# Optimization experiments

Measured on AMD Instinct MI355X. Metric: run time of the kernel, lower is better.

Reference implementation:

```python
import jax, jax.numpy as jnp
import numpy as np

N = 131072
F_IN = 256
FEATURES = 64
N_SOURCES = 32


def setup_inputs() -> dict:
    key = jax.random.key(0)
    k1, k2, k3 = jax.random.split(key, 3)
    x = jax.random.normal(k1, (N, F_IN), dtype=jnp.float32)
    source = jax.random.randint(k2, (N,), 0, N_SOURCES, dtype=jnp.int32)
    W = jax.random.normal(k3, (F_IN, N_SOURCES * FEATURES), dtype=jnp.float32) * (1.0 / np.sqrt(F_IN))
    b = jnp.zeros((N_SOURCES * FEATURES,), dtype=jnp.float32)
    return {"x": x, "source": source, "W": W, "b": b}


def reference(x, source, W, b):
    # Dense projection to all sources: (N, n_sources*features)
    y = jnp.dot(x, W) + b
    # Per-row gather of the slice belonging to this row's source id.
    # Equivalent to y[i, source[i]*FEATURES : (source[i]+1)*FEATURES].
    y = y.reshape(x.shape[0], N_SOURCES, FEATURES)
    out = jnp.take_along_axis(y, source[:, None, None].astype(jnp.int32), axis=1)
    return out[:, 0, :]  # (N, FEATURES)
```

## Files before the change

### kernel.cpp

```cpp
#include <hip/hip_runtime.h>

#define N_ROWS   131072
#define F_IN     256
#define FEAT     64
#define NSRC     32
#define WSTRIDE  (NSRC * FEAT)
#define NCH      32
#define CHUNK    4096
#define LCAP     320
#define NBUCK    (NCH * NSRC)
#define KPAD     264
#define TPAD     66
#define TR       32

#define MCHUNK   4096
#define LCAP1    512

typedef __attribute__((ext_vector_type(8))) short  bf16x8;
typedef __attribute__((ext_vector_type(4))) float  f32x4;

__device__ __forceinline__ unsigned short f2bf(float f) {
    union { float f; unsigned u; } c; c.f = f;
    unsigned r = c.u + 0x7fffu + ((c.u >> 16) & 1u);
    return (unsigned short)(r >> 16);
}

__device__ __forceinline__ bf16x8 pack8(f32x4 f0, f32x4 f1) {
    bf16x8 a;
    a[0] = (short)f2bf(f0[0]); a[1] = (short)f2bf(f0[1]);
    a[2] = (short)f2bf(f0[2]); a[3] = (short)f2bf(f0[3]);
    a[4] = (short)f2bf(f1[0]); a[5] = (short)f2bf(f1[1]);
    a[6] = (short)f2bf(f1[2]); a[7] = (short)f2bf(f1[3]);
    return a;
}

__global__ void zero_counts(int* __restrict__ ws) {
    const int i = blockIdx.x * 256 + threadIdx.x;
    if (i < NBUCK) ws[i] = 0;
}

__global__ __launch_bounds__(256)
void compact_kernel(const int* __restrict__ src, int* __restrict__ ws) {
    __shared__ int lcnt[NSRC];
    __shared__ int gbase[NSRC];
    const int tid = threadIdx.x;
    if (tid < NSRC) lcnt[tid] = 0;
    __syncthreads();
    const int row = blockIdx.x * 256 + tid;
    const int s   = src[row];
    const int c   = blockIdx.x >> 4;
    const int p   = atomicAdd(&lcnt[s], 1);
    __syncthreads();
    if (tid < NSRC && lcnt[tid] > 0)
        gbase[tid] = atomicAdd(&ws[c * NSRC + tid], lcnt[tid]);
    __syncthreads();
    const int pos = gbase[s] + p;
    if (pos < LCAP)
        ws[NBUCK + ((size_t)(c * NSRC + s)) * LCAP + pos] = row;
}

__device__ __forceinline__ void load_tile(const float* __restrict__ x,
                                          const int* lst, int count, int tile,
                                          int row8, int p, f32x4 av[8]) {
    const int gi  = min(tile * TR + row8, count - 1);
    const int row = lst[gi];
    const float* rp = x + (size_t)row * F_IN + p * 4;
    #pragma unroll
    for (int i = 0; i < 8; ++i)
        av[i] = *(const f32x4*)(rp + i * 32);
}

__device__ __forceinline__ void write_tile(unsigned short* XsBuf,
                                           int row8, int p, const f32x4 av[8]) {
    #pragma unroll
    for (int i = 0; i < 8; ++i) {
        unsigned lo = (unsigned)f2bf(av[i][0]) | ((unsigned)f2bf(av[i][1]) << 16);
        unsigned hi = (unsigned)f2bf(av[i][2]) | ((unsigned)f2bf(av[i][3]) << 16);
        unsigned* d = (unsigned*)&XsBuf[row8 * KPAD + i * 32 + p * 4];
        d[0] = lo; d[1] = hi;
    }
}

__device__ __forceinline__ void tile_compute(
    const unsigned short* __restrict__ XsBuf, const unsigned short* __restrict__ Wt,
    float* __restrict__ T, const int* __restrict__ lst,
    float bias0, float bias1, float* __restrict__ out,
    int tile, int count, int w, int lane, int col, int quad, int mh, int nh) {

    f32x4 acc0 = (f32x4){0.f, 0.f, 0.f, 0.f};
    f32x4 acc1 = (f32x4){0.f, 0.f, 0.f, 0.f};
    #pragma unroll
    for (int kk = 0; kk < 8; ++kk) {
        const bf16x8 a = *(const bf16x8*)&XsBuf[(mh * 16 + col) * KPAD + kk * 32 + quad * 8];
        const bf16x8 b0 = *(const bf16x8*)&Wt[(nh * 32 + col) * KPAD + kk * 32 + quad * 8];
        const bf16x8 b1 = *(const bf16x8*)&Wt[(nh * 32 + 16 + col) * KPAD + kk * 32 + quad * 8];
        acc0 = __builtin_amdgcn_mfma_f32_16x16x32_bf16(a, b0, acc0, 0, 0, 0);
        acc1 = __builtin_amdgcn_mfma_f32_16x16x32_bf16(a, b1, acc1, 0, 0, 0);
    }
    #pragma unroll
    for (int reg = 0; reg < 4; ++reg) {
        T[(mh * 16 + quad * 4 + reg) * TPAD + nh * 32 + col]      = acc0[reg] + bias0;
        T[(mh * 16 + quad * 4 + reg) * TPAD + nh * 32 + 16 + col] = acc1[reg] + bias1;
    }
    __syncthreads();
    #pragma unroll
    for (int r = 0; r < 8; ++r) {
        const int lr = w * 8 + r;
        const int gi = tile * TR + lr;
        if (gi < count) {
            const int grow = lst[gi];
            out[(size_t)grow * FEAT + lane] = T[lr * TPAD + lane];
        }
    }
}

__global__ __launch_bounds__(256, 2)
void gemm_kernel(const float* __restrict__ x, const float* __restrict__ W,
                 const float* __restrict__ b, const int* __restrict__ ws,
                 float* __restrict__ out) {
    __shared__ __align__(16) unsigned short Wt[FEAT * KPAD];
    __shared__ __align__(16) unsigned short Xs[2][TR * KPAD];
    __shared__ __align__(16) float T[TR * TPAD];
    __shared__ int lst[LCAP];

    const int tid    = threadIdx.x;
    const int c      = blockIdx.x;
    const int s      = blockIdx.y;
    const int bucket = c * NSRC + s;
    const int count  = min(ws[bucket], LCAP);
    if (count == 0) return;

    const int* gl = ws + NBUCK + (size_t)bucket * LCAP;
    for (int i = tid; i < count; i += 256) lst[i] = gl[i];

    {
        const int n  = tid & 63;
        const int kp = (tid >> 6) * 2;
        #pragma unroll
        for (int k0 = 0; k0 < F_IN; k0 += 8) {
            const int k = k0 + kp;
            const float w0 = W[(size_t)k       * WSTRIDE + s * FEAT + n];
            const float w1 = W[(size_t)(k + 1) * WSTRIDE + s * FEAT + n];
            *(unsigned*)&Wt[n * KPAD + k] = (unsigned)f2bf(w0) | ((unsigned)f2bf(w1) << 16);
        }
    }

    const int lane = tid & 63, w = tid >> 6;
    const int col  = lane & 15, quad = lane >> 4;
    const int mh   = w & 1,    nh   = w >> 1;
    const int row8 = tid >> 3, p    = tid & 7;

    const float bias0 = b[s * FEAT + nh * 32 + col];
    const float bias1 = b[s * FEAT + nh * 32 + 16 + col];

    __syncthreads();

    const int ntiles = (count + TR - 1) / TR;
    f32x4 avA[8], avB[8];
    load_tile(x, lst, count, 0, row8, p, avA);

    for (int t = 0; t < ntiles; t += 2) {
        write_tile(Xs[0], row8, p, avA);
        if (t + 1 < ntiles) load_tile(x, lst, count, t + 1, row8, p, avB);
        __syncthreads();
        tile_compute(Xs[0], Wt, T, lst, bias0, bias1, out,
                     t, count, w, lane, col, quad, mh, nh);
        if (t + 1 >= ntiles) break;

        write_tile(Xs[1], row8, p, avB);
        if (t + 2 < ntiles) load_tile(x, lst, count, t + 2, row8, p, avA);
        __syncthreads();
        tile_compute(Xs[1], Wt, T, lst, bias0, bias1, out,
                     t + 1, count, w, lane, col, quad, mh, nh);
    }
}

__global__ __launch_bounds__(256, 4)
void mono_kernel(const float* __restrict__ x, const int* __restrict__ src,
                 const float* __restrict__ W, const float* __restrict__ b,
                 float* __restrict__ out) {
    __shared__ __align__(16) unsigned short Wt[FEAT * KPAD];
    __shared__ int lst[LCAP1];
    __shared__ int cnt;
    const int tid = threadIdx.x, s = blockIdx.y, chunk0 = blockIdx.x * MCHUNK;
    if (tid == 0) cnt = 0;
    __syncthreads();
    {
        const int n = tid & 63, kp = (tid >> 6) * 2;
        #pragma unroll
        for (int k0 = 0; k0 < F_IN; k0 += 8) {
            const int k = k0 + kp;
            const float w0 = W[(size_t)k * WSTRIDE + s * FEAT + n];
            const float w1 = W[(size_t)(k + 1) * WSTRIDE + s * FEAT + n];
            *(unsigned*)&Wt[n * KPAD + k] = (unsigned)f2bf(w0) | ((unsigned)f2bf(w1) << 16);
        }
    }
    #pragma unroll
    for (int r = 0; r < MCHUNK / 256; ++r) {
        const int row = chunk0 + r * 256 + tid;
        if (src[row] == s) {
            const int p = atomicAdd(&cnt, 1);
            if (p < LCAP1) lst[p] = row;
        }
    }
    __syncthreads();
    const int count = cnt;
    if (count == 0) return;
    const int lane = tid & 63, w = tid >> 6, col = lane & 15, quad = lane >> 4;
    float bias[4];
    #pragma unroll
    for (int nt = 0; nt < 4; ++nt) bias[nt] = b[s * FEAT + nt * 16 + col];
    const int npass = (count + 63) >> 6;
    for (int pp = 0; pp < npass; ++pp) {
        const int base = pp * 64 + w * 16;
        const int ia = lst[min(base + col, count - 1)];
        const float* ap = x + (size_t)ia * F_IN + quad * 8;
        f32x4 av[16];
        #pragma unroll
        for (int kk = 0; kk < 8; ++kk) {
            av[2 * kk]     = *(const f32x4*)(ap + kk * 32);
            av[2 * kk + 1] = *(const f32x4*)(ap + kk * 32 + 4);
        }
        f32x4 acc[4];
        #pragma unroll
        for (int nt = 0; nt < 4; ++nt) acc[nt] = (f32x4){0.f, 0.f, 0.f, 0.f};
        #pragma unroll
        for (int kk = 0; kk < 8; ++kk) {
            const bf16x8 a = pack8(av[2 * kk], av[2 * kk + 1]);
            #pragma unroll
            for (int nt = 0; nt < 4; ++nt) {
                const bf16x8 bb = *(const bf16x8*)&Wt[(nt * 16 + col) * KPAD + kk * 32 + quad * 8];
                acc[nt] = __builtin_amdgcn_mfma_f32_16x16x32_bf16(a, bb, acc[nt], 0, 0, 0);
            }
        }
        #pragma unroll
        for (int reg = 0; reg < 4; ++reg) {
            const int gm = base + quad * 4 + reg;
            if (gm < count) {
                const int row = lst[gm];
                float* op = out + (size_t)row * FEAT;
                #pragma unroll
                for (int nt = 0; nt < 4; ++nt)
                    op[nt * 16 + col] = acc[nt][reg] + bias[nt];
            }
        }
    }
}

extern "C" void kernel_launch(void* const* d_in, const int* in_sizes, int n_in,
                              void* d_out, int out_size, void* d_ws, size_t ws_size,
                              hipStream_t stream) {
    const float* x   = (const float*)d_in[0];
    const int*   src = (const int*)d_in[1];
    const float* W   = (const float*)d_in[2];
    const float* b   = (const float*)d_in[3];
    float*       out = (float*)d_out;

    const size_t ws_needed = (size_t)NBUCK * (1 + LCAP) * sizeof(int);
    if (ws_size >= ws_needed) {
        int* ws = (int*)d_ws;
        zero_counts<<<dim3(4), dim3(256), 0, stream>>>(ws);
        compact_kernel<<<dim3(N_ROWS / 256), dim3(256), 0, stream>>>(src, ws);
        gemm_kernel<<<dim3(NCH, NSRC), dim3(256), 0, stream>>>(x, W, b, ws, out);
    } else {
        mono_kernel<<<dim3(N_ROWS / MCHUNK, NSRC), dim3(256), 0, stream>>>(x, src, W, b, out);
    }
}
```

Before: 220.3 us.

## Fuse bucketing and grouped GEMM into a single kernel with wave-ballot compaction

Replaces the three-kernel pipeline (zero counts, global compaction into workspace buckets, tiled GEMM) with one kernel per (source, chunk) block. Each block scans its chunk's source ids itself, compacts matching rows with a wave ballot plus popcount and one shared atomic per wave, then has each wave process its own 16-row tiles straight from registers without LDS staging of X. This removes two launches and the workspace round trip. In exchange every block rereads 4096 source ids, which is 32x redundant reading of src, and it drops the double-buffered X prefetch. The row cap stays at 320, which relies on each bucket's size staying near its expected average of 128.

```diff
diff --git a/kernel.cpp b/kernel.cpp
--- a/kernel.cpp
+++ b/kernel.cpp
@@ -5,16 +5,10 @@
 #define FEAT     64
 #define NSRC     32
 #define WSTRIDE  (NSRC * FEAT)
-#define NCH      32
 #define CHUNK    4096
+#define NCH      (N_ROWS / CHUNK)
 #define LCAP     320
-#define NBUCK    (NCH * NSRC)
 #define KPAD     264
-#define TPAD     66
-#define TR       32
-
-#define MCHUNK   4096
-#define LCAP1    512
 
 typedef __attribute__((ext_vector_type(8))) short  bf16x8;
 typedef __attribute__((ext_vector_type(4))) float  f32x4;
@@ -34,104 +28,38 @@
     return a;
 }
 
-__global__ void zero_counts(int* __restrict__ ws) {
-    const int i = blockIdx.x * 256 + threadIdx.x;
-    if (i < NBUCK) ws[i] = 0;
-}
+__global__ __launch_bounds__(256, 3)
+void fused_kernel(const float* __restrict__ x, const int* __restrict__ src,
+                  const float* __restrict__ W, const float* __restrict__ b,
+                  float* __restrict__ out) {
+    __shared__ __align__(16) unsigned short Wt[FEAT * KPAD];
+    __shared__ int lst[LCAP];
+    __shared__ int cnt;
 
-__global__ __launch_bounds__(256)
-void compact_kernel(const int* __restrict__ src, int* __restrict__ ws) {
-    __shared__ int lcnt[NSRC];
-    __shared__ int gbase[NSRC];
     const int tid = threadIdx.x;
-    if (tid < NSRC) lcnt[tid] = 0;
+    const int s   = blockIdx.x;
+    const int c   = blockIdx.y;
+
+    if (tid == 0) cnt = 0;
     __syncthreads();
-    const int row = blockIdx.x * 256 + tid;
-    const int s   = src[row];
-    const int c   = blockIdx.x >> 4;
-    const int p   = atomicAdd(&lcnt[s], 1);
-    __syncthreads();
-    if (tid < NSRC && lcnt[tid] > 0)
-        gbase[tid] = atomicAdd(&ws[c * NSRC + tid], lcnt[tid]);
-    __syncthreads();
-    const int pos = gbase[s] + p;
-    if (pos < LCAP)
-        ws[NBUCK + ((size_t)(c * NSRC + s)) * LCAP + pos] = row;
-}
 
-__device__ __forceinline__ void load_tile(const float* __restrict__ x,
-                                          const int* lst, int count, int tile,
-                                          int row8, int p, f32x4 av[8]) {
-    const int gi  = min(tile * TR + row8, count - 1);
-    const int row = lst[gi];
-    const float* rp = x + (size_t)row * F_IN + p * 4;
-    #pragma unroll
-    for (int i = 0; i < 8; ++i)
-        av[i] = *(const f32x4*)(rp + i * 32);
-}
-
-__device__ __forceinline__ void write_tile(unsigned short* XsBuf,
-                                           int row8, int p, const f32x4 av[8]) {
-    #pragma unroll
-    for (int i = 0; i < 8; ++i) {
-        unsigned lo = (unsigned)f2bf(av[i][0]) | ((unsigned)f2bf(av[i][1]) << 16);
-        unsigned hi = (unsigned)f2bf(av[i][2]) | ((unsigned)f2bf(av[i][3]) << 16);
-        unsigned* d = (unsigned*)&XsBuf[row8 * KPAD + i * 32 + p * 4];
-        d[0] = lo; d[1] = hi;
-    }
-}
-
-__device__ __forceinline__ void tile_compute(
-    const unsigned short* __restrict__ XsBuf, const unsigned short* __restrict__ Wt,
-    float* __restrict__ T, const int* __restrict__ lst,
-    float bias0, float bias1, float* __restrict__ out,
-    int tile, int count, int w, int lane, int col, int quad, int mh, int nh) {
-
-    f32x4 acc0 = (f32x4){0.f, 0.f, 0.f, 0.f};
-    f32x4 acc1 = (f32x4){0.f, 0.f, 0.f, 0.f};
-    #pragma unroll
-    for (int kk = 0; kk < 8; ++kk) {
-        const bf16x8 a = *(const bf16x8*)&XsBuf[(mh * 16 + col) * KPAD + kk * 32 + quad * 8];
-        const bf16x8 b0 = *(const bf16x8*)&Wt[(nh * 32 + col) * KPAD + kk * 32 + quad * 8];
-        const bf16x8 b1 = *(const bf16x8*)&Wt[(nh * 32 + 16 + col) * KPAD + kk * 32 + quad * 8];
-        acc0 = __builtin_amdgcn_mfma_f32_16x16x32_bf16(a, b0, acc0, 0, 0, 0);
-        acc1 = __builtin_amdgcn_mfma_f32_16x16x32_bf16(a, b1, acc1, 0, 0, 0);
-    }
-    #pragma unroll
-    for (int reg = 0; reg < 4; ++reg) {
-        T[(mh * 16 + quad * 4 + reg) * TPAD + nh * 32 + col]      = acc0[reg] + bias0;
-        T[(mh * 16 + quad * 4 + reg) * TPAD + nh * 32 + 16 + col] = acc1[reg] + bias1;
-    }
-    __syncthreads();
-    #pragma unroll
-    for (int r = 0; r < 8; ++r) {
-        const int lr = w * 8 + r;
-        const int gi = tile * TR + lr;
-        if (gi < count) {
-            const int grow = lst[gi];
-            out[(size_t)grow * FEAT + lane] = T[lr * TPAD + lane];
+    {
+        const unsigned long long below = (1ull << (tid & 63)) - 1ull;
+        #pragma unroll
+        for (int it = 0; it < CHUNK / 256; ++it) {
+            const int row = c * CHUNK + it * 256 + tid;
+            const bool m = (src[row] == s);
+            const unsigned long long mask = __ballot(m);
+            int wbase = 0;
+            if ((tid & 63) == 0)
+                wbase = atomicAdd(&cnt, (int)__popcll(mask));
+            wbase = __shfl(wbase, 0);
+            if (m) {
+                const int pos = wbase + (int)__popcll(mask & below);
+                if (pos < LCAP) lst[pos] = row;
+            }
         }
     }
-}
-
-__global__ __launch_bounds__(256, 2)
-void gemm_kernel(const float* __restrict__ x, const float* __restrict__ W,
-                 const float* __restrict__ b, const int* __restrict__ ws,
-                 float* __restrict__ out) {
-    __shared__ __align__(16) unsigned short Wt[FEAT * KPAD];
-    __shared__ __align__(16) unsigned short Xs[2][TR * KPAD];
-    __shared__ __align__(16) float T[TR * TPAD];
-    __shared__ int lst[LCAP];
-
-    const int tid    = threadIdx.x;
-    const int c      = blockIdx.x;
-    const int s      = blockIdx.y;
-    const int bucket = c * NSRC + s;
-    const int count  = min(ws[bucket], LCAP);
-    if (count == 0) return;
-
-    const int* gl = ws + NBUCK + (size_t)bucket * LCAP;
-    for (int i = tid; i < count; i += 256) lst[i] = gl[i];
 
     {
         const int n  = tid & 63;
@@ -145,85 +73,34 @@
         }
     }
 
+    __syncthreads();
+    const int count = min(cnt, LCAP);
+    if (count == 0) return;
+
     const int lane = tid & 63, w = tid >> 6;
     const int col  = lane & 15, quad = lane >> 4;
-    const int mh   = w & 1,    nh   = w >> 1;
-    const int row8 = tid >> 3, p    = tid & 7;
 
-    const float bias0 = b[s * FEAT + nh * 32 + col];
-    const float bias1 = b[s * FEAT + nh * 32 + 16 + col];
-
-    __syncthreads();
-
-    const int ntiles = (count + TR - 1) / TR;
-    f32x4 avA[8], avB[8];
-    load_tile(x, lst, count, 0, row8, p, avA);
-
-    for (int t = 0; t < ntiles; t += 2) {
-        write_tile(Xs[0], row8, p, avA);
-        if (t + 1 < ntiles) load_tile(x, lst, count, t + 1, row8, p, avB);
-        __syncthreads();
-        tile_compute(Xs[0], Wt, T, lst, bias0, bias1, out,
-                     t, count, w, lane, col, quad, mh, nh);
-        if (t + 1 >= ntiles) break;
-
-        write_tile(Xs[1], row8, p, avB);
-        if (t + 2 < ntiles) load_tile(x, lst, count, t + 2, row8, p, avA);
-        __syncthreads();
-        tile_compute(Xs[1], Wt, T, lst, bias0, bias1, out,
-                     t + 1, count, w, lane, col, quad, mh, nh);
-    }
-}
-
-__global__ __launch_bounds__(256, 4)
-void mono_kernel(const float* __restrict__ x, const int* __restrict__ src,
-                 const float* __restrict__ W, const float* __restrict__ b,
-                 float* __restrict__ out) {
-    __shared__ __align__(16) unsigned short Wt[FEAT * KPAD];
-    __shared__ int lst[LCAP1];
-    __shared__ int cnt;
-    const int tid = threadIdx.x, s = blockIdx.y, chunk0 = blockIdx.x * MCHUNK;
-    if (tid == 0) cnt = 0;
-    __syncthreads();
-    {
-        const int n = tid & 63, kp = (tid >> 6) * 2;
-        #pragma unroll
-        for (int k0 = 0; k0 < F_IN; k0 += 8) {
-            const int k = k0 + kp;
-            const float w0 = W[(size_t)k * WSTRIDE + s * FEAT + n];
-            const float w1 = W[(size_t)(k + 1) * WSTRIDE + s * FEAT + n];
-            *(unsigned*)&Wt[n * KPAD + k] = (unsigned)f2bf(w0) | ((unsigned)f2bf(w1) << 16);
-        }
-    }
-    #pragma unroll
-    for (int r = 0; r < MCHUNK / 256; ++r) {
-        const int row = chunk0 + r * 256 + tid;
-        if (src[row] == s) {
-            const int p = atomicAdd(&cnt, 1);
-            if (p < LCAP1) lst[p] = row;
-        }
-    }
-    __syncthreads();
-    const int count = cnt;
-    if (count == 0) return;
-    const int lane = tid & 63, w = tid >> 6, col = lane & 15, quad = lane >> 4;
     float bias[4];
     #pragma unroll
     for (int nt = 0; nt < 4; ++nt) bias[nt] = b[s * FEAT + nt * 16 + col];
-    const int npass = (count + 63) >> 6;
-    for (int pp = 0; pp < npass; ++pp) {
-        const int base = pp * 64 + w * 16;
-        const int ia = lst[min(base + col, count - 1)];
-        const float* ap = x + (size_t)ia * F_IN + quad * 8;
+
+    const int ntiles = (count + 15) >> 4;
+    for (int t = w; t < ntiles; t += 4) {
+        const int tb = t * 16;
+        const int arow = lst[min(tb + col, count - 1)];
+        const float* rp = x + (size_t)arow * F_IN + quad * 8;
+
         f32x4 av[16];
         #pragma unroll
         for (int kk = 0; kk < 8; ++kk) {
-            av[2 * kk]     = *(const f32x4*)(ap + kk * 32);
-            av[2 * kk + 1] = *(const f32x4*)(ap + kk * 32 + 4);
+            av[2 * kk]     = *(const f32x4*)(rp + kk * 32);
+            av[2 * kk + 1] = *(const f32x4*)(rp + kk * 32 + 4);
         }
+
         f32x4 acc[4];
         #pragma unroll
         for (int nt = 0; nt < 4; ++nt) acc[nt] = (f32x4){0.f, 0.f, 0.f, 0.f};
+
         #pragma unroll
         for (int kk = 0; kk < 8; ++kk) {
             const bf16x8 a = pack8(av[2 * kk], av[2 * kk + 1]);
@@ -233,15 +110,16 @@
                 acc[nt] = __builtin_amdgcn_mfma_f32_16x16x32_bf16(a, bb, acc[nt], 0, 0, 0);
             }
         }
+
         #pragma unroll
         for (int reg = 0; reg < 4; ++reg) {
-            const int gm = base + quad * 4 + reg;
+            const int gm = tb + quad * 4 + reg;
             if (gm < count) {
-                const int row = lst[gm];
-                float* op = out + (size_t)row * FEAT;
+                const int grow = lst[gm];
+                float* op = out + (size_t)grow * FEAT + col;
                 #pragma unroll
                 for (int nt = 0; nt < 4; ++nt)
-                    op[nt * 16 + col] = acc[nt][reg] + bias[nt];
+                    op[nt * 16] = acc[nt][reg] + bias[nt];
             }
         }
     }
@@ -256,13 +134,5 @@
     const float* b   = (const float*)d_in[3];
     float*       out = (float*)d_out;
 
-    const size_t ws_needed = (size_t)NBUCK * (1 + LCAP) * sizeof(int);
-    if (ws_size >= ws_needed) {
-        int* ws = (int*)d_ws;
-        zero_counts<<<dim3(4), dim3(256), 0, stream>>>(ws);
-        compact_kernel<<<dim3(N_ROWS / 256), dim3(256), 0, stream>>>(src, ws);
-        gemm_kernel<<<dim3(NCH, NSRC), dim3(256), 0, stream>>>(x, W, b, ws, out);
-    } else {
-        mono_kernel<<<dim3(N_ROWS / MCHUNK, NSRC), dim3(256), 0, stream>>>(x, src, W, b, out);
-    }
+    fused_kernel<<<dim3(NSRC, NCH), dim3(256), 0, stream>>>(x, src, W, b, out);
 }
```

Result: slower. 244.1 us (+10.8%).

## Gather rows directly into MFMA registers per wave, drop LDS staging and syncs

Applied to the files above, without the earlier changes.

The gemm kernel no longer stages gathered x rows through shared memory. Each wave now independently gathers 16-row tiles straight into registers in the MFMA A-operand layout, packs them to bf16, and computes all 64 output columns, storing results directly from accumulators. This removes the block-wide barriers, the LDS X/T buffers and the transpose round-trip, and each wave prefetches its next tile into registers. The grid dimensions are also swapped so blocks for the same chunk run adjacently. The cost is higher register pressure (32 f32x4 buffers), uncoalesced 16-wide output stores, and lost overlap inside the block when some waves have no tiles.

```diff
diff --git a/kernel.cpp b/kernel.cpp
--- a/kernel.cpp
+++ b/kernel.cpp
@@ -10,8 +10,6 @@
 #define LCAP     320
 #define NBUCK    (NCH * NSRC)
 #define KPAD     264
-#define TPAD     66
-#define TR       32
 
 #define MCHUNK   4096
 #define LCAP1    512
@@ -59,57 +57,43 @@
         ws[NBUCK + ((size_t)(c * NSRC + s)) * LCAP + pos] = row;
 }
 
-__device__ __forceinline__ void load_tile(const float* __restrict__ x,
-                                          const int* lst, int count, int tile,
-                                          int row8, int p, f32x4 av[8]) {
-    const int gi  = min(tile * TR + row8, count - 1);
-    const int row = lst[gi];
-    const float* rp = x + (size_t)row * F_IN + p * 4;
-    #pragma unroll
-    for (int i = 0; i < 8; ++i)
-        av[i] = *(const f32x4*)(rp + i * 32);
-}
-
-__device__ __forceinline__ void write_tile(unsigned short* XsBuf,
-                                           int row8, int p, const f32x4 av[8]) {
-    #pragma unroll
-    for (int i = 0; i < 8; ++i) {
-        unsigned lo = (unsigned)f2bf(av[i][0]) | ((unsigned)f2bf(av[i][1]) << 16);
-        unsigned hi = (unsigned)f2bf(av[i][2]) | ((unsigned)f2bf(av[i][3]) << 16);
-        unsigned* d = (unsigned*)&XsBuf[row8 * KPAD + i * 32 + p * 4];
-        d[0] = lo; d[1] = hi;
-    }
-}
-
-__device__ __forceinline__ void tile_compute(
-    const unsigned short* __restrict__ XsBuf, const unsigned short* __restrict__ Wt,
-    float* __restrict__ T, const int* __restrict__ lst,
-    float bias0, float bias1, float* __restrict__ out,
-    int tile, int count, int w, int lane, int col, int quad, int mh, int nh) {
-
-    f32x4 acc0 = (f32x4){0.f, 0.f, 0.f, 0.f};
-    f32x4 acc1 = (f32x4){0.f, 0.f, 0.f, 0.f};
+__device__ __forceinline__ void gather16(const float* __restrict__ x,
+                                         const int* lst, int count, int tile,
+                                         int col, int quad, f32x4 av[16]) {
+    const int arow = lst[min(tile * 16 + col, count - 1)];
+    const float* rp = x + (size_t)arow * F_IN + quad * 8;
     #pragma unroll
     for (int kk = 0; kk < 8; ++kk) {
-        const bf16x8 a = *(const bf16x8*)&XsBuf[(mh * 16 + col) * KPAD + kk * 32 + quad * 8];
-        const bf16x8 b0 = *(const bf16x8*)&Wt[(nh * 32 + col) * KPAD + kk * 32 + quad * 8];
-        const bf16x8 b1 = *(const bf16x8*)&Wt[(nh * 32 + 16 + col) * KPAD + kk * 32 + quad * 8];
-        acc0 = __builtin_amdgcn_mfma_f32_16x16x32_bf16(a, b0, acc0, 0, 0, 0);
-        acc1 = __builtin_amdgcn_mfma_f32_16x16x32_bf16(a, b1, acc1, 0, 0, 0);
+        av[2 * kk]     = *(const f32x4*)(rp + kk * 32);
+        av[2 * kk + 1] = *(const f32x4*)(rp + kk * 32 + 4);
+    }
+}
+
+__device__ __forceinline__ void compute_store16(
+    const f32x4 av[16], const unsigned short* __restrict__ Wt,
+    const int* lst, const float bias[4], float* __restrict__ out,
+    int tile, int count, int col, int quad) {
+    f32x4 acc[4];
+    #pragma unroll
+    for (int nt = 0; nt < 4; ++nt) acc[nt] = (f32x4){0.f, 0.f, 0.f, 0.f};
+    #pragma unroll
+    for (int kk = 0; kk < 8; ++kk) {
+        const bf16x8 a = pack8(av[2 * kk], av[2 * kk + 1]);
+        #pragma unroll
+        for (int nt = 0; nt < 4; ++nt) {
+            const bf16x8 bb = *(const bf16x8*)&Wt[(nt * 16 + col) * KPAD + kk * 32 + quad * 8];
+            acc[nt] = __builtin_amdgcn_mfma_f32_16x16x32_bf16(a, bb, acc[nt], 0, 0, 0);
+        }
     }
     #pragma unroll
     for (int reg = 0; reg < 4; ++reg) {
-        T[(mh * 16 + quad * 4 + reg) * TPAD + nh * 32 + col]      = acc0[reg] + bias0;
-        T[(mh * 16 + quad * 4 + reg) * TPAD + nh * 32 + 16 + col] = acc1[reg] + bias1;
-    }
-    __syncthreads();
-    #pragma unroll
-    for (int r = 0; r < 8; ++r) {
-        const int lr = w * 8 + r;
-        const int gi = tile * TR + lr;
-        if (gi < count) {
-            const int grow = lst[gi];
-            out[(size_t)grow * FEAT + lane] = T[lr * TPAD + lane];
+        const int gm = tile * 16 + quad * 4 + reg;
+        if (gm < count) {
+            const int grow = lst[gm];
+            float* op = out + (size_t)grow * FEAT + col;
+            #pragma unroll
+            for (int nt = 0; nt < 4; ++nt)
+                op[nt * 16] = acc[nt][reg] + bias[nt];
         }
     }
 }
@@ -119,13 +103,11 @@
                  const float* __restrict__ b, const int* __restrict__ ws,
                  float* __restrict__ out) {
     __shared__ __align__(16) unsigned short Wt[FEAT * KPAD];
-    __shared__ __align__(16) unsigned short Xs[2][TR * KPAD];
-    __shared__ __align__(16) float T[TR * TPAD];
     __shared__ int lst[LCAP];
 
     const int tid    = threadIdx.x;
-    const int c      = blockIdx.x;
-    const int s      = blockIdx.y;
+    const int s      = blockIdx.x;
+    const int c      = blockIdx.y;
     const int bucket = c * NSRC + s;
     const int count  = min(ws[bucket], LCAP);
     if (count == 0) return;
@@ -145,33 +127,30 @@
         }
     }
 
+    __syncthreads();
+
     const int lane = tid & 63, w = tid >> 6;
     const int col  = lane & 15, quad = lane >> 4;
-    const int mh   = w & 1,    nh   = w >> 1;
-    const int row8 = tid >> 3, p    = tid & 7;
-
-    const float bias0 = b[s * FEAT + nh * 32 + col];
-    const float bias1 = b[s * FEAT + nh * 32 + 16 + col];
-
-    __syncthreads();
-
-    const int ntiles = (count + TR - 1) / TR;
-    f32x4 avA[8], avB[8];
-    load_tile(x, lst, count, 0, row8, p, avA);
-
-    for (int t = 0; t < ntiles; t += 2) {
-        write_tile(Xs[0], row8, p, avA);
-        if (t + 1 < ntiles) load_tile(x, lst, count, t + 1, row8, p, avB);
-        __syncthreads();
-        tile_compute(Xs[0], Wt, T, lst, bias0, bias1, out,
-                     t, count, w, lane, col, quad, mh, nh);
-        if (t + 1 >= ntiles) break;
-
-        write_tile(Xs[1], row8, p, avB);
-        if (t + 2 < ntiles) load_tile(x, lst, count, t + 2, row8, p, avA);
-        __syncthreads();
-        tile_compute(Xs[1], Wt, T, lst, bias0, bias1, out,
-                     t + 1, count, w, lane, col, quad, mh, nh);
+
+    float bias[4];
+    #pragma unroll
+    for (int nt = 0; nt < 4; ++nt) bias[nt] = b[s * FEAT + nt * 16 + col];
+
+    const int ntiles = (count + 15) >> 4;
+    if (w >= ntiles) return;
+
+    f32x4 avA[16], avB[16];
+    gather16(x, lst, count, w, col, quad, avA);
+    for (int t = w; ; ) {
+        const int t1 = t + 4;
+        if (t1 < ntiles) gather16(x, lst, count, t1, col, quad, avB);
+        compute_store16(avA, Wt, lst, bias, out, t, count, col, quad);
+        if (t1 >= ntiles) break;
+        const int t2 = t + 8;
+        if (t2 < ntiles) gather16(x, lst, count, t2, col, quad, avA);
+        compute_store16(avB, Wt, lst, bias, out, t1, count, col, quad);
+        if (t2 >= ntiles) break;
+        t = t2;
     }
 }
 
@@ -261,7 +240,7 @@
         int* ws = (int*)d_ws;
         zero_counts<<<dim3(4), dim3(256), 0, stream>>>(ws);
         compact_kernel<<<dim3(N_ROWS / 256), dim3(256), 0, stream>>>(src, ws);
-        gemm_kernel<<<dim3(NCH, NSRC), dim3(256), 0, stream>>>(x, W, b, ws, out);
+        gemm_kernel<<<dim3(NSRC, NCH), dim3(256), 0, stream>>>(x, W, b, ws, out);
     } else {
         mono_kernel<<<dim3(N_ROWS / MCHUNK, NSRC), dim3(256), 0, stream>>>(x, src, W, b, out);
     }
```

New measurement: 235.7 us. 1.07x slower.
